# Kernel tuning notes

Measured on AMD Instinct MI355X. Metric: run time of the kernel, lower is better.

The kernel has to match this reference:

```python
import jax, jax.numpy as jnp
import numpy as np

N_NODES = 100000
N_EDGES = 800000
HID = 128
N_LAYERS = 3
N_GRAPHS = 64
LN_EPS = 1e-5


def setup_inputs() -> dict:
    key = jax.random.key(0)
    ks = jax.random.split(key, 12)
    s = 1.0 / np.sqrt(HID)  # xavier-ish scale
    return {
        "node_features": jax.random.normal(ks[0], (N_NODES, HID), jnp.float32),
        "edge_attr": jax.random.normal(ks[1], (N_EDGES, HID), jnp.float32),
        "in_proj_w": jax.random.normal(ks[2], (HID, HID), jnp.float32) * s,
        "in_proj_b": jnp.zeros((HID,), jnp.float32),
        "gcn_w": jax.random.normal(ks[3], (N_LAYERS, HID, HID), jnp.float32) * s,
        "gcn_ew": jax.random.normal(ks[4], (N_LAYERS, HID, HID), jnp.float32) * s,
        "gcn_b": jnp.zeros((N_LAYERS, HID), jnp.float32),
        "ln_scale": jnp.ones((N_LAYERS, HID), jnp.float32),
        "ln_bias": jnp.zeros((N_LAYERS, HID), jnp.float32),
        "out_proj_w": jax.random.normal(ks[5], (HID, HID), jnp.float32) * s,
        "out_proj_b": jnp.zeros((HID,), jnp.float32),
        "edge_index": jax.random.randint(ks[6], (2, N_EDGES), 0, N_NODES, jnp.int64),
        "batch": jnp.sort(jax.random.randint(ks[7], (N_NODES,), 0, N_GRAPHS, jnp.int64)),
    }


def _layer_norm(x, scale, bias):
    m = jnp.mean(x, axis=-1, keepdims=True)
    v = jnp.mean(jnp.square(x - m), axis=-1, keepdims=True)
    return (x - m) * jax.lax.rsqrt(v + LN_EPS) * scale + bias


def reference(node_features, edge_attr, in_proj_w, in_proj_b, gcn_w, gcn_ew,
              gcn_b, ln_scale, ln_bias, out_proj_w, out_proj_b,
              edge_index, batch):
    src, dst = edge_index[0], edge_index[1]
    x = node_features @ in_proj_w + in_proj_b  # [N, HID]
    for i in range(N_LAYERS):
        residual = x
        h = x @ gcn_w[i]                       # [N, HID]
        ew = edge_attr @ gcn_ew[i]             # [E, HID] edge gate
        msgs = h[src] * ew                     # [E, HID] gather + gate
        agg = jax.ops.segment_sum(msgs, dst, num_segments=N_NODES)  # scatter-add
        h = jax.nn.relu(agg + gcn_b[i])
        # dropout is identity in eval mode
        if i > 0:
            h = h + residual
        x = _layer_norm(h, ln_scale[i], ln_bias[i])
    x = x @ out_proj_w + out_proj_b            # [N, HID]
    # global mean pool per graph
    sums = jax.ops.segment_sum(x, batch, num_segments=N_GRAPHS)
    counts = jax.ops.segment_sum(jnp.ones((N_NODES,), x.dtype), batch,
                                 num_segments=N_GRAPHS)
    return sums / jnp.maximum(counts, 1.0)[:, None]  # [N_GRAPHS, HID]
```

## Files before the change

### kernel.cpp

```cpp
#include <hip/hip_runtime.h>

#define HID 128

typedef __attribute__((ext_vector_type(8))) short bf16x8;
typedef __attribute__((ext_vector_type(4))) float f32x4;
typedef __attribute__((ext_vector_type(4))) unsigned short u16x4;

__device__ __forceinline__ unsigned short f2bf(float f) {
  union { float f; unsigned u; } v; v.f = f;
  return (unsigned short)((v.u + 0x7FFFu + ((v.u >> 16) & 1u)) >> 16);
}
__device__ __forceinline__ float bf2f(unsigned short h) {
  union { unsigned u; float f; } v; v.u = ((unsigned)h) << 16; return v.f;
}


template<bool SRCF32, bool BIAS, bool OUTBF16>
__global__ __launch_bounds__(256, 3) void gemm_node_kernel(
    const void* __restrict__ Xv, const unsigned short* __restrict__ Wt,
    const float* __restrict__ bias, float* __restrict__ Yf,
    unsigned short* __restrict__ Yb, int nrows)
{
  const int tid  = threadIdx.x;
  const int lane = tid & 63;
  const int wave = tid >> 6;
  const int lr = lane & 15;
  const int lg = lane >> 4;
  const long row0 = (long)blockIdx.x * 128 + wave * 32;

  bf16x8 A[2][4];
  #pragma unroll
  for (int rt = 0; rt < 2; ++rt) {
    long R = row0 + rt * 16 + lr;
    if (R >= nrows) R = nrows - 1;
    if (SRCF32) {
      const float* xp = (const float*)Xv + R * HID;
      #pragma unroll
      for (int ks = 0; ks < 4; ++ks) {
        float4 lo = *(const float4*)(xp + ks * 32 + lg * 8);
        float4 hi = *(const float4*)(xp + ks * 32 + lg * 8 + 4);
        bf16x8 a;
        a[0] = (short)f2bf(lo.x); a[1] = (short)f2bf(lo.y);
        a[2] = (short)f2bf(lo.z); a[3] = (short)f2bf(lo.w);
        a[4] = (short)f2bf(hi.x); a[5] = (short)f2bf(hi.y);
        a[6] = (short)f2bf(hi.z); a[7] = (short)f2bf(hi.w);
        A[rt][ks] = a;
      }
    } else {
      const unsigned short* xp = (const unsigned short*)Xv + R * HID;
      #pragma unroll
      for (int ks = 0; ks < 4; ++ks)
        A[rt][ks] = *(const bf16x8*)(xp + ks * 32 + lg * 8);
    }
  }

  f32x4 acc[2][8];
  #pragma unroll
  for (int rt = 0; rt < 2; ++rt)
    #pragma unroll
    for (int ct = 0; ct < 8; ++ct)
      acc[rt][ct] = (f32x4){0.f, 0.f, 0.f, 0.f};

  #pragma unroll
  for (int ks = 0; ks < 4; ++ks) {
    bf16x8 Bf[8];
    #pragma unroll
    for (int ct = 0; ct < 8; ++ct)
      Bf[ct] = *(const bf16x8*)(Wt + (ct * 16 + lr) * HID + ks * 32 + lg * 8);
    #pragma unroll
    for (int rt = 0; rt < 2; ++rt)
      #pragma unroll
      for (int ct = 0; ct < 8; ++ct)
        acc[rt][ct] = __builtin_amdgcn_mfma_f32_16x16x32_bf16(
            A[rt][ks], Bf[ct], acc[rt][ct], 0, 0, 0);
  }

  #pragma unroll
  for (int rt = 0; rt < 2; ++rt) {
    #pragma unroll
    for (int r = 0; r < 4; ++r) {
      long e = row0 + rt * 16 + lg * 4 + r;
      if (e < nrows) {
        if (OUTBF16) {
          bf16x8 o;
          #pragma unroll
          for (int ct = 0; ct < 8; ++ct) {
            float v = acc[rt][ct][r];
            if (BIAS) v += bias[ct * 16 + lr];
            o[ct] = (short)f2bf(v);
          }
          *(bf16x8*)(Yb + e * HID + lr * 8) = o;
        } else {
          #pragma unroll
          for (int ct = 0; ct < 8; ++ct) {
            int col = ct * 16 + lr;
            float v = acc[rt][ct][r];
            if (BIAS) v += bias[col];
            Yf[e * HID + col] = v;
          }
        }
      }
    }
  }
}

__global__ __launch_bounds__(256, 3) void tri_edge_gemm_kernel(
    const float* __restrict__ EA, const int* __restrict__ perm,
    const unsigned short* __restrict__ Wt,
    unsigned short* __restrict__ msgs, int nE)
{
  __shared__ unsigned short sA[128 * 144];
  __shared__ int sPerm[128];
  const int tid  = threadIdx.x;
  const int lane = tid & 63;
  const int wave = tid >> 6;
  const int lr = lane & 15;
  const int lg = lane >> 4;
  const long row0 = (long)blockIdx.x * 128;

  if (tid < 128) sPerm[tid] = perm[row0 + tid];
  __syncthreads();

  #pragma unroll
  for (int i = 0; i < 16; ++i) {
    int idx = tid + i * 256;
    int row = idx >> 5, part = idx & 31;
    const float* xp = EA + (long)sPerm[row] * HID + part * 4;
    float4 v = *(const float4*)xp;
    u16x4 o;
    o[0] = f2bf(v.x); o[1] = f2bf(v.y); o[2] = f2bf(v.z); o[3] = f2bf(v.w);
    *(u16x4*)(sA + row * 144 + part * 4) = o;
  }
  __syncthreads();

  bf16x8 A[2][4];
  #pragma unroll
  for (int rt = 0; rt < 2; ++rt) {
    int rl = wave * 32 + rt * 16 + lr;
    #pragma unroll
    for (int ks = 0; ks < 4; ++ks)
      A[rt][ks] = *(const bf16x8*)(sA + rl * 144 + ks * 32 + lg * 8);
  }

  #pragma unroll 1
  for (int w = 0; w < 3; ++w) {
    const unsigned short* Wp = Wt + (size_t)w * 16384;
    unsigned short* Mp = msgs + (size_t)w * nE * HID;

    f32x4 acc[2][8];
    #pragma unroll
    for (int rt = 0; rt < 2; ++rt)
      #pragma unroll
      for (int ct = 0; ct < 8; ++ct)
        acc[rt][ct] = (f32x4){0.f, 0.f, 0.f, 0.f};

    #pragma unroll
    for (int ks = 0; ks < 4; ++ks) {
      bf16x8 Bf[8];
      #pragma unroll
      for (int ct = 0; ct < 8; ++ct)
        Bf[ct] = *(const bf16x8*)(Wp + (ct * 16 + lr) * HID + ks * 32 + lg * 8);
      #pragma unroll
      for (int rt = 0; rt < 2; ++rt)
        #pragma unroll
        for (int ct = 0; ct < 8; ++ct)
          acc[rt][ct] = __builtin_amdgcn_mfma_f32_16x16x32_bf16(
              A[rt][ks], Bf[ct], acc[rt][ct], 0, 0, 0);
    }

    #pragma unroll
    for (int rt = 0; rt < 2; ++rt) {
      #pragma unroll
      for (int r = 0; r < 4; ++r) {
        long e = row0 + wave * 32 + rt * 16 + lg * 4 + r;
        bf16x8 o;
        #pragma unroll
        for (int ct = 0; ct < 8; ++ct) o[ct] = (short)f2bf(acc[rt][ct][r]);
        *(bf16x8*)(Mp + e * HID + lr * 8) = o;
      }
    }
  }
}

__global__ __launch_bounds__(128) void seg_ln_kernel(
    const unsigned short* __restrict__ msgs, const unsigned short* __restrict__ Hb,
    const int* __restrict__ ssrc, const int* __restrict__ segend,
    const float* __restrict__ b, const float* __restrict__ lnS,
    const float* __restrict__ lnB, const float* res,
    float* __restrict__ xf, unsigned short* __restrict__ xb)
{
  __shared__ float2 red[2][8];
  const int t = threadIdx.x;
  const int w = t >> 6;
  const int lane = t & 63;
  const int dbase = blockIdx.x * 8;

  const float bb = b[t];
  const float sc = lnS[t];
  const float sb = lnB[t];

  int p = (dbase == 0) ? 0 : segend[dbase - 1];
  #pragma unroll 1
  for (int j = 0; j < 8; ++j) {
    const long node = dbase + j;
    const int end = segend[node];
    float a0 = 0.f, a1 = 0.f;
    int q = p;
    for (; q + 1 < end; q += 2) {
      int s0 = ssrc[q];
      int s1 = ssrc[q + 1];
      float m0 = bf2f(msgs[(long)q * HID + t]);
      float h0 = bf2f(Hb[(long)s0 * HID + t]);
      float m1 = bf2f(msgs[(long)(q + 1) * HID + t]);
      float h1 = bf2f(Hb[(long)s1 * HID + t]);
      a0 += m0 * h0;
      a1 += m1 * h1;
    }
    if (q < end) {
      int s = ssrc[q];
      a0 += bf2f(msgs[(long)q * HID + t]) * bf2f(Hb[(long)s * HID + t]);
    }
    p = end;

    float v = fmaxf(a0 + a1 + bb, 0.f);
    if (res != nullptr) v += res[node * HID + t];

    float s = v, qq = v * v;
    #pragma unroll
    for (int off = 32; off >= 1; off >>= 1) {
      s  += __shfl_xor(s, off);
      qq += __shfl_xor(qq, off);
    }
    if (lane == 0) red[w][j] = make_float2(s, qq);
    __syncthreads();
    float2 t0 = red[0][j], t1 = red[1][j];
    float S = t0.x + t1.x, Q = t0.y + t1.y;
    float mean = S * (1.f / 128.f);
    float var = Q * (1.f / 128.f) - mean * mean;
    float rstd = rsqrtf(var + 1e-5f);
    float o = (v - mean) * rstd * sc + sb;
    xf[node * HID + t] = o;
    xb[node * HID + t] = f2bf(o);
  }
}

__global__ __launch_bounds__(256, 3) void gemm_edge_fb_kernel(
    const float* __restrict__ EA, const int* __restrict__ perm,
    const unsigned short* __restrict__ Wt, const unsigned short* __restrict__ Hb,
    const int* __restrict__ ssrc, const int* __restrict__ sdst,
    float* __restrict__ agg, int nE)
{
  const int tid  = threadIdx.x;
  const int lane = tid & 63;
  const int wave = tid >> 6;
  const int lr = lane & 15;
  const int lg = lane >> 4;
  const long row0 = (long)blockIdx.x * 128 + wave * 32;

  bf16x8 A[2][4];
  #pragma unroll
  for (int rt = 0; rt < 2; ++rt) {
    long R = row0 + rt * 16 + lr;
    const float* xp = EA + (long)perm[R] * HID;
    #pragma unroll
    for (int ks = 0; ks < 4; ++ks) {
      float4 lo = *(const float4*)(xp + ks * 32 + lg * 8);
      float4 hi = *(const float4*)(xp + ks * 32 + lg * 8 + 4);
      bf16x8 a;
      a[0] = (short)f2bf(lo.x); a[1] = (short)f2bf(lo.y);
      a[2] = (short)f2bf(lo.z); a[3] = (short)f2bf(lo.w);
      a[4] = (short)f2bf(hi.x); a[5] = (short)f2bf(hi.y);
      a[6] = (short)f2bf(hi.z); a[7] = (short)f2bf(hi.w);
      A[rt][ks] = a;
    }
  }

  f32x4 acc[2][8];
  #pragma unroll
  for (int rt = 0; rt < 2; ++rt)
    #pragma unroll
    for (int ct = 0; ct < 8; ++ct)
      acc[rt][ct] = (f32x4){0.f, 0.f, 0.f, 0.f};

  #pragma unroll
  for (int ks = 0; ks < 4; ++ks) {
    bf16x8 Bf[8];
    #pragma unroll
    for (int ct = 0; ct < 8; ++ct)
      Bf[ct] = *(const bf16x8*)(Wt + (ct * 16 + lr) * HID + ks * 32 + lg * 8);
    #pragma unroll
    for (int rt = 0; rt < 2; ++rt)
      #pragma unroll
      for (int ct = 0; ct < 8; ++ct)
        acc[rt][ct] = __builtin_amdgcn_mfma_f32_16x16x32_bf16(
            A[rt][ks], Bf[ct], acc[rt][ct], 0, 0, 0);
  }

  #pragma unroll
  for (int rt = 0; rt < 2; ++rt) {
    const long base = row0 + rt * 16 + lg * 4;
    int4 sv = *(const int4*)(ssrc + base);
    int4 dv = *(const int4*)(sdst + base);
    bf16x8 hv0 = *(const bf16x8*)(Hb + (long)sv.x * HID + lr * 8);
    bf16x8 hv1 = *(const bf16x8*)(Hb + (long)sv.y * HID + lr * 8);
    bf16x8 hv2 = *(const bf16x8*)(Hb + (long)sv.z * HID + lr * 8);
    bf16x8 hv3 = *(const bf16x8*)(Hb + (long)sv.w * HID + lr * 8);

    float am[8];
    #pragma unroll
    for (int ct = 0; ct < 8; ++ct)
      am[ct] = acc[rt][ct][0] * bf2f((unsigned short)hv0[ct]);
    int dprev = dv.x;
    {
      bool same = (dv.y == dprev);
      if (!same) {
        float* ap = agg + (long)dprev * HID + lr;
        #pragma unroll
        for (int ct = 0; ct < 8; ++ct) atomicAdd(ap + ct * 16, am[ct]);
      }
      #pragma unroll
      for (int ct = 0; ct < 8; ++ct) {
        float m = acc[rt][ct][1] * bf2f((unsigned short)hv1[ct]);
        am[ct] = same ? am[ct] + m : m;
      }
      dprev = dv.y;
    }
    {
      bool same = (dv.z == dprev);
      if (!same) {
        float* ap = agg + (long)dprev * HID + lr;
        #pragma unroll
        for (int ct = 0; ct < 8; ++ct) atomicAdd(ap + ct * 16, am[ct]);
      }
      #pragma unroll
      for (int ct = 0; ct < 8; ++ct) {
        float m = acc[rt][ct][2] * bf2f((unsigned short)hv2[ct]);
        am[ct] = same ? am[ct] + m : m;
      }
      dprev = dv.z;
    }
    {
      bool same = (dv.w == dprev);
      if (!same) {
        float* ap = agg + (long)dprev * HID + lr;
        #pragma unroll
        for (int ct = 0; ct < 8; ++ct) atomicAdd(ap + ct * 16, am[ct]);
      }
      #pragma unroll
      for (int ct = 0; ct < 8; ++ct) {
        float m = acc[rt][ct][3] * bf2f((unsigned short)hv3[ct]);
        am[ct] = same ? am[ct] + m : m;
      }
      dprev = dv.w;
    }
    float* ap = agg + (long)dprev * HID + lr;
    #pragma unroll
    for (int ct = 0; ct < 8; ++ct) atomicAdd(ap + ct * 16, am[ct]);
  }
}

__global__ void hist_kernel(const int* __restrict__ dst, int nE,
                            int* __restrict__ hist)
{
  int i = blockIdx.x * 256 + threadIdx.x;
  if (i < nE) atomicAdd(&hist[dst[i]], 1);
}

__global__ __launch_bounds__(256) void scan1_kernel(
    const int* __restrict__ hist, int n, int* __restrict__ partial)
{
  __shared__ int buf[256];
  int t = threadIdx.x;
  int i = blockIdx.x * 256 + t;
  buf[t] = (i < n) ? hist[i] : 0;
  __syncthreads();
  #pragma unroll
  for (int off = 128; off >= 1; off >>= 1) {
    if (t < off) buf[t] += buf[t + off];
    __syncthreads();
  }
  if (t == 0) partial[blockIdx.x] = buf[0];
}

__global__ __launch_bounds__(512) void scan2_kernel(int* __restrict__ partial,
                                                    int nb)
{
  __shared__ int buf[512];
  int t = threadIdx.x;
  buf[t] = (t < nb) ? partial[t] : 0;
  __syncthreads();
  for (int off = 1; off < 512; off <<= 1) {
    int v = (t >= off) ? buf[t - off] : 0;
    __syncthreads();
    buf[t] += v;
    __syncthreads();
  }
  if (t < nb) partial[t] = (t == 0) ? 0 : buf[t - 1];
}

__global__ __launch_bounds__(256) void scan3_kernel(
    const int* __restrict__ hist, const int* __restrict__ partial,
    int* __restrict__ cursor, int n)
{
  __shared__ int buf[256];
  int t = threadIdx.x;
  int i = blockIdx.x * 256 + t;
  int v = (i < n) ? hist[i] : 0;
  buf[t] = v;
  __syncthreads();
  for (int off = 1; off < 256; off <<= 1) {
    int w = (t >= off) ? buf[t - off] : 0;
    __syncthreads();
    buf[t] += w;
    __syncthreads();
  }
  if (i < n) cursor[i] = partial[blockIdx.x] + buf[t] - v;
}

__global__ void scatter_kernel(const int* __restrict__ src,
                               const int* __restrict__ dst, int nE,
                               int* __restrict__ cursor,
                               int* __restrict__ perm,
                               int* __restrict__ ssrc, int* __restrict__ sdst)
{
  int e = blockIdx.x * 256 + threadIdx.x;
  if (e < nE) {
    int d = dst[e];
    int pos = atomicAdd(&cursor[d], 1);
    perm[pos] = e;
    ssrc[pos] = src[e];
    sdst[pos] = d;
  }
}

__global__ __launch_bounds__(256) void prep_w_kernel(
    const float* __restrict__ ipw, const float* __restrict__ gw,
    const float* __restrict__ gew, const float* __restrict__ opw,
    unsigned short* __restrict__ wt)
{
  int idx = blockIdx.x * 1024 + threadIdx.x * 4;
  #pragma unroll
  for (int t = 0; t < 4; ++t) {
    int i = idx + t;
    int m = i >> 14, r = i & 16383;
    int n = r >> 7, k = r & 127;
    const float* srcm;
    bool kperm;
    if (m == 0)      { srcm = ipw; kperm = false; }
    else if (m <= 3) { srcm = gw  + (size_t)(m - 1) * 16384; kperm = true; }
    else if (m <= 6) { srcm = gew + (size_t)(m - 4) * 16384; kperm = false; }
    else             { srcm = opw; kperm = true; }
    int kk = kperm ? ((k & 7) * 16 + (k >> 3)) : k;
    wt[i] = f2bf(srcm[kk * HID + n]);
  }
}

__global__ void prep_params_kernel(const float* __restrict__ gb,
                                   const float* __restrict__ lns,
                                   const float* __restrict__ lnb,
                                   float* __restrict__ bp,
                                   float* __restrict__ lsp,
                                   float* __restrict__ lbp)
{
  int idx = threadIdx.x + blockIdx.x * 128;
  if (idx < 384) {
    int i = idx >> 7, p = idx & 127;
    int c = (p & 7) * 16 + (p >> 3);
    bp[idx]  = gb[i * 128 + c];
    lsp[idx] = lns[i * 128 + c];
    lbp[idx] = lnb[i * 128 + c];
  }
}

__global__ __launch_bounds__(256) void ln_nat_kernel(
    const float* __restrict__ agg, const float* __restrict__ b,
    const float* res, const float* __restrict__ lnS,
    const float* __restrict__ lnB, float* xf, unsigned short* __restrict__ xb,
    int n)
{
  const int wave = threadIdx.x >> 6;
  const int lane = threadIdx.x & 63;
  const long node = (long)blockIdx.x * 4 + wave;
  if (node >= n) return;

  float2 v = *(const float2*)&agg[node * HID + lane * 2];
  float2 bb = *(const float2*)&b[lane * 2];
  v.x += bb.x; v.y += bb.y;
  v.x = fmaxf(v.x, 0.f); v.y = fmaxf(v.y, 0.f);
  if (res != nullptr) {
    float2 rr = *(const float2*)&res[node * HID + lane * 2];
    v.x += rr.x; v.y += rr.y;
  }
  float s = v.x + v.y;
  #pragma unroll
  for (int off = 32; off >= 1; off >>= 1) s += __shfl_xor(s, off);
  float mean = s * (1.f / 128.f);
  float dx = v.x - mean, dy = v.y - mean;
  float q = dx * dx + dy * dy;
  #pragma unroll
  for (int off = 32; off >= 1; off >>= 1) q += __shfl_xor(q, off);
  float rstd = rsqrtf(q * (1.f / 128.f) + 1e-5f);
  float2 sc = *(const float2*)&lnS[lane * 2];
  float2 sb = *(const float2*)&lnB[lane * 2];
  float ox = dx * rstd * sc.x + sb.x;
  float oy = dy * rstd * sc.y + sb.y;
  *(float2*)&xf[node * HID + lane * 2] = make_float2(ox, oy);
  int c0 = lane * 2, c1 = lane * 2 + 1;
  xb[node * HID + ((c0 & 15) * 8 + (c0 >> 4))] = f2bf(ox);
  xb[node * HID + ((c1 & 15) * 8 + (c1 >> 4))] = f2bf(oy);
}

__global__ void graph_count_kernel(const int* __restrict__ batch, int n,
                                   int nG, int* __restrict__ counts)
{
  int g = threadIdx.x;
  if (g >= nG) return;
  int lo0 = 0, hi0 = n;
  while (lo0 < hi0) { int mid = (lo0 + hi0) >> 1; if (batch[mid] < g) lo0 = mid + 1; else hi0 = mid; }
  int lo1 = lo0, hi1 = n;
  while (lo1 < hi1) { int mid = (lo1 + hi1) >> 1; if (batch[mid] < g + 1) lo1 = mid + 1; else hi1 = mid; }
  counts[g] = lo1 - lo0;
}

__global__ __launch_bounds__(128) void pool_kernel(
    const float* __restrict__ X, const int* __restrict__ batch, int n,
    float* __restrict__ sums)
{
  const int col = threadIdx.x;
  long n0 = (long)blockIdx.x * 64;
  long n1 = n0 + 64; if (n1 > n) n1 = n;
  if (n0 >= n) return;
  float s = 0.f;
  int g = batch[n0];
  for (long i = n0; i < n1; ++i) {
    int gi = batch[i];
    if (gi != g) {
      atomicAdd(&sums[g * HID + col], s);
      s = 0.f;
      g = gi;
    }
    s += X[i * HID + col];
  }
  atomicAdd(&sums[g * HID + col], s);
}

__global__ void finalize_kernel(const float* __restrict__ sums,
                                const int* __restrict__ counts,
                                float* __restrict__ out, int total)
{
  int i = blockIdx.x * 256 + threadIdx.x;
  if (i < total) {
    int g = i >> 7;
    float c = (float)counts[g];
    out[i] = sums[i] / fmaxf(c, 1.f);
  }
}

extern "C" void kernel_launch(void* const* d_in, const int* in_sizes, int n_in,
                              void* d_out, int out_size, void* d_ws, size_t ws_size,
                              hipStream_t stream)
{
  const float* nf    = (const float*)d_in[0];
  const float* ea    = (const float*)d_in[1];
  const float* ipw   = (const float*)d_in[2];
  const float* ipb   = (const float*)d_in[3];
  const float* gw    = (const float*)d_in[4];
  const float* gew   = (const float*)d_in[5];
  const float* gb    = (const float*)d_in[6];
  const float* lns   = (const float*)d_in[7];
  const float* lnb   = (const float*)d_in[8];
  const float* opw   = (const float*)d_in[9];
  const float* opb   = (const float*)d_in[10];
  const int*   ei    = (const int*)d_in[11];
  const int*   batch = (const int*)d_in[12];
  float* out = (float*)d_out;

  const int N = 100000;
  const int E = 800000;
  const int G = 64;
  const int* srcI = ei;
  const int* dstI = ei + E;

  char* ws = (char*)d_ws;
  const size_t nodeF = (size_t)N * HID * sizeof(float);
  const size_t nodeB = (size_t)N * HID * sizeof(unsigned short);
  size_t off = 0;
  float*          xf   = (float*)(ws + off); off += nodeF;
  float*          agg  = (float*)(ws + off); off += nodeF;
  unsigned short* xb   = (unsigned short*)(ws + off); off += nodeB;
  unsigned short* hb   = (unsigned short*)(ws + off); off += nodeB;
  unsigned short* wt   = (unsigned short*)(ws + off); off += 8 * 16384 * 2;
  float*          bp   = (float*)(ws + off); off += 384 * 4;
  float*          lsp  = (float*)(ws + off); off += 384 * 4;
  float*          lbp  = (float*)(ws + off); off += 384 * 4;
  int*            perm = (int*)(ws + off); off += (size_t)E * 4;
  int*            ssrc = (int*)(ws + off); off += (size_t)E * 4;
  int*            sdst = (int*)(ws + off); off += (size_t)E * 4;
  int*            hist = (int*)(ws + off); off += (size_t)N * 4;
  int*            curs = (int*)(ws + off); off += (size_t)N * 4;
  int*            part = (int*)(ws + off); off += 512 * 4;
  float*          sums = (float*)(ws + off); off += (size_t)G * HID * 4;
  int*            cnts = (int*)(ws + off); off += G * 4;
  unsigned short* msgs = (unsigned short*)(ws + off);
  off += 3 * (size_t)E * HID * sizeof(unsigned short);
  const bool hoisted = (ws_size >= off);

  dim3 blk(256);
  const int nBlkN = (N + 127) / 128;
  const int nBlkE = E / 128;
  const int nBins = (N + 255) / 256;

  prep_w_kernel<<<128, blk, 0, stream>>>(ipw, gw, gew, opw, wt);
  prep_params_kernel<<<3, dim3(128), 0, stream>>>(gb, lns, lnb, bp, lsp, lbp);

  hipMemsetAsync(hist, 0, (size_t)N * 4, stream);
  hist_kernel<<<(E + 255) / 256, blk, 0, stream>>>(dstI, E, hist);
  scan1_kernel<<<nBins, blk, 0, stream>>>(hist, N, part);
  scan2_kernel<<<1, dim3(512), 0, stream>>>(part, nBins);
  scan3_kernel<<<nBins, blk, 0, stream>>>(hist, part, curs, N);
  scatter_kernel<<<(E + 255) / 256, blk, 0, stream>>>(srcI, dstI, E, curs,
                                                      perm, ssrc, sdst);

  if (hoisted) {
    tri_edge_gemm_kernel<<<nBlkE, blk, 0, stream>>>(
        ea, perm, wt + (size_t)4 * 16384, msgs, E);
  }

  gemm_node_kernel<true, true, true><<<nBlkN, blk, 0, stream>>>(
      nf, wt, ipb, nullptr, xb, N);

  for (int i = 0; i < 3; ++i) {
    gemm_node_kernel<false, false, true><<<nBlkN, blk, 0, stream>>>(
        xb, wt + (size_t)(1 + i) * 16384, nullptr, nullptr, hb, N);
    if (hoisted) {
      seg_ln_kernel<<<N / 8, dim3(128), 0, stream>>>(
          msgs + (size_t)i * E * HID, hb, ssrc, curs,
          bp + i * HID, lsp + i * HID, lbp + i * HID,
          (i > 0) ? xf : nullptr, xf, xb);
    } else {
      hipMemsetAsync(agg, 0, nodeF, stream);
      gemm_edge_fb_kernel<<<nBlkE, blk, 0, stream>>>(
          ea, perm, wt + (size_t)(4 + i) * 16384, hb, ssrc, sdst, agg, E);
      ln_nat_kernel<<<(N + 3) / 4, blk, 0, stream>>>(
          agg, gb + i * HID, (i > 0) ? xf : nullptr, lns + i * HID,
          lnb + i * HID, xf, xb, N);
    }
  }

  gemm_node_kernel<false, true, false><<<nBlkN, blk, 0, stream>>>(
      xb, wt + (size_t)7 * 16384, opb, agg, nullptr, N);

  graph_count_kernel<<<1, dim3(64), 0, stream>>>(batch, N, G, cnts);
  hipMemsetAsync(sums, 0, (size_t)G * HID * 4, stream);
  pool_kernel<<<(N + 63) / 64, dim3(128), 0, stream>>>(agg, batch, N, sums);
  finalize_kernel<<<(G * HID + 255) / 256, blk, 0, stream>>>(
      sums, cnts, out, G * HID);
}
```

Measured before the change: 1.025 ms.

## Process one node per wavefront in seg_ln with packed bf16 pairs, batch edge loads

The segment-sum plus layernorm kernel now gives each node to a single 64-lane wavefront, with every lane handling two adjacent features through 32-bit packed bf16 loads and stores. This removes the shared-memory reduction and the per-node __syncthreads. Each block now covers 32 nodes with 256 threads. The tri-edge GEMM staging loop issues eight gathered float4 loads before converting them, to raise memory-level parallelism, and its launch bound asks for 4 blocks per SM. Register pressure in the GEMM could increase, and the seg_ln grid now assumes N is divisible by 32.

Measured after the change: 1.063 ms. 1.04x slower.

```diff
diff --git a/kernel.cpp b/kernel.cpp
--- a/kernel.cpp
+++ b/kernel.cpp
@@ -12,6 +12,12 @@
 }
 __device__ __forceinline__ float bf2f(unsigned short h) {
   union { unsigned u; float f; } v; v.u = ((unsigned)h) << 16; return v.f;
+}
+__device__ __forceinline__ float bf2f_lo(unsigned u) {
+  union { unsigned u; float f; } v; v.u = u << 16; return v.f;
+}
+__device__ __forceinline__ float bf2f_hi(unsigned u) {
+  union { unsigned u; float f; } v; v.u = u & 0xffff0000u; return v.f;
 }
 
 
@@ -104,7 +110,7 @@
   }
 }
 
-__global__ __launch_bounds__(256, 3) void tri_edge_gemm_kernel(
+__global__ __launch_bounds__(256, 4) void tri_edge_gemm_kernel(
     const float* __restrict__ EA, const int* __restrict__ perm,
     const unsigned short* __restrict__ Wt,
     unsigned short* __restrict__ msgs, int nE)
@@ -122,14 +128,22 @@
   __syncthreads();
 
   #pragma unroll
-  for (int i = 0; i < 16; ++i) {
-    int idx = tid + i * 256;
-    int row = idx >> 5, part = idx & 31;
-    const float* xp = EA + (long)sPerm[row] * HID + part * 4;
-    float4 v = *(const float4*)xp;
-    u16x4 o;
-    o[0] = f2bf(v.x); o[1] = f2bf(v.y); o[2] = f2bf(v.z); o[3] = f2bf(v.w);
-    *(u16x4*)(sA + row * 144 + part * 4) = o;
+  for (int c = 0; c < 2; ++c) {
+    float4 v[8];
+    int row[8], part[8];
+    #pragma unroll
+    for (int i = 0; i < 8; ++i) {
+      int idx = tid + (c * 8 + i) * 256;
+      row[i] = idx >> 5; part[i] = idx & 31;
+      v[i] = *(const float4*)(EA + (long)sPerm[row[i]] * HID + part[i] * 4);
+    }
+    #pragma unroll
+    for (int i = 0; i < 8; ++i) {
+      u16x4 o;
+      o[0] = f2bf(v[i].x); o[1] = f2bf(v[i].y);
+      o[2] = f2bf(v[i].z); o[3] = f2bf(v[i].w);
+      *(u16x4*)(sA + row[i] * 144 + part[i] * 4) = o;
+    }
   }
   __syncthreads();
 
@@ -182,65 +196,70 @@
   }
 }
 
-__global__ __launch_bounds__(128) void seg_ln_kernel(
+__global__ __launch_bounds__(256) void seg_ln_kernel(
     const unsigned short* __restrict__ msgs, const unsigned short* __restrict__ Hb,
     const int* __restrict__ ssrc, const int* __restrict__ segend,
     const float* __restrict__ b, const float* __restrict__ lnS,
     const float* __restrict__ lnB, const float* res,
     float* __restrict__ xf, unsigned short* __restrict__ xb)
 {
-  __shared__ float2 red[2][8];
-  const int t = threadIdx.x;
-  const int w = t >> 6;
-  const int lane = t & 63;
-  const int dbase = blockIdx.x * 8;
-
-  const float bb = b[t];
-  const float sc = lnS[t];
-  const float sb = lnB[t];
+  const int lane = threadIdx.x & 63;
+  const int wave = threadIdx.x >> 6;
+  const int dbase = blockIdx.x * 32 + wave * 8;
+  const int c = lane * 2;
+
+  const float2 bb = *(const float2*)&b[c];
+  const float2 sc = *(const float2*)&lnS[c];
+  const float2 sb = *(const float2*)&lnB[c];
 
   int p = (dbase == 0) ? 0 : segend[dbase - 1];
   #pragma unroll 1
   for (int j = 0; j < 8; ++j) {
     const long node = dbase + j;
     const int end = segend[node];
-    float a0 = 0.f, a1 = 0.f;
+    float a00 = 0.f, a01 = 0.f, a10 = 0.f, a11 = 0.f;
     int q = p;
     for (; q + 1 < end; q += 2) {
       int s0 = ssrc[q];
       int s1 = ssrc[q + 1];
-      float m0 = bf2f(msgs[(long)q * HID + t]);
-      float h0 = bf2f(Hb[(long)s0 * HID + t]);
-      float m1 = bf2f(msgs[(long)(q + 1) * HID + t]);
-      float h1 = bf2f(Hb[(long)s1 * HID + t]);
-      a0 += m0 * h0;
-      a1 += m1 * h1;
+      unsigned m0 = *(const unsigned*)(msgs + (long)q * HID + c);
+      unsigned h0 = *(const unsigned*)(Hb + (long)s0 * HID + c);
+      unsigned m1 = *(const unsigned*)(msgs + (long)(q + 1) * HID + c);
+      unsigned h1 = *(const unsigned*)(Hb + (long)s1 * HID + c);
+      a00 += bf2f_lo(m0) * bf2f_lo(h0);
+      a01 += bf2f_hi(m0) * bf2f_hi(h0);
+      a10 += bf2f_lo(m1) * bf2f_lo(h1);
+      a11 += bf2f_hi(m1) * bf2f_hi(h1);
     }
     if (q < end) {
       int s = ssrc[q];
-      a0 += bf2f(msgs[(long)q * HID + t]) * bf2f(Hb[(long)s * HID + t]);
+      unsigned m = *(const unsigned*)(msgs + (long)q * HID + c);
+      unsigned h = *(const unsigned*)(Hb + (long)s * HID + c);
+      a00 += bf2f_lo(m) * bf2f_lo(h);
+      a01 += bf2f_hi(m) * bf2f_hi(h);
     }
     p = end;
 
-    float v = fmaxf(a0 + a1 + bb, 0.f);
-    if (res != nullptr) v += res[node * HID + t];
-
-    float s = v, qq = v * v;
+    float v0 = fmaxf(a00 + a10 + bb.x, 0.f);
+    float v1 = fmaxf(a01 + a11 + bb.y, 0.f);
+    if (res != nullptr) {
+      float2 rr = *(const float2*)&res[node * HID + c];
+      v0 += rr.x; v1 += rr.y;
+    }
+    float s = v0 + v1, qq = v0 * v0 + v1 * v1;
     #pragma unroll
     for (int off = 32; off >= 1; off >>= 1) {
       s  += __shfl_xor(s, off);
       qq += __shfl_xor(qq, off);
     }
-    if (lane == 0) red[w][j] = make_float2(s, qq);
-    __syncthreads();
-    float2 t0 = red[0][j], t1 = red[1][j];
-    float S = t0.x + t1.x, Q = t0.y + t1.y;
-    float mean = S * (1.f / 128.f);
-    float var = Q * (1.f / 128.f) - mean * mean;
+    float mean = s * (1.f / 128.f);
+    float var = qq * (1.f / 128.f) - mean * mean;
     float rstd = rsqrtf(var + 1e-5f);
-    float o = (v - mean) * rstd * sc + sb;
-    xf[node * HID + t] = o;
-    xb[node * HID + t] = f2bf(o);
+    float o0 = (v0 - mean) * rstd * sc.x + sb.x;
+    float o1 = (v1 - mean) * rstd * sc.y + sb.y;
+    *(float2*)&xf[node * HID + c] = make_float2(o0, o1);
+    unsigned pk = (unsigned)f2bf(o0) | ((unsigned)f2bf(o1) << 16);
+    *(unsigned*)&xb[node * HID + c] = pk;
   }
 }
 
@@ -633,7 +652,7 @@
     gemm_node_kernel<false, false, true><<<nBlkN, blk, 0, stream>>>(
         xb, wt + (size_t)(1 + i) * 16384, nullptr, nullptr, hb, N);
     if (hoisted) {
-      seg_ln_kernel<<<N / 8, dim3(128), 0, stream>>>(
+      seg_ln_kernel<<<N / 32, blk, 0, stream>>>(
           msgs + (size_t)i * E * HID, hb, ssrc, curs,
           bp + i * HID, lsp + i * HID, lbp + i * HID,
           (i > 0) ? xf : nullptr, xf, xb);
```
